# Kernel optimization log

Measured on AMD Instinct MI355X. Metric: run time of the kernel, lower is better.

Reference implementation:

```python
import jax, jax.numpy as jnp
import numpy as np

B, N, T = 64, 100, 100
FS, F, STRIDE = 3, 16, 1  # filter_size, num_filters, stride
DENSITY = 0.05


def setup_inputs() -> dict:
    key = jax.random.key(0)
    k1, k2, k3, k4 = jax.random.split(key, 4)
    vals = jax.random.uniform(k1, (B, N, N, T), dtype=jnp.float32, minval=0.01, maxval=1.0)
    mask = jax.random.uniform(k2, (B, N, N, T)) < DENSITY
    x = jnp.where(mask, vals, 0.0)
    # learned params, matching tf.random_normal_initializer(stddev=0.05)
    w = 0.05 * jax.random.normal(k3, (N * N * FS, F), dtype=jnp.float32)
    gammat = 0.05 * jax.random.normal(k4, (1, 1), dtype=jnp.float32)
    return {"x": x, "w": w, "gammat": gammat}


def reference(x, w, gammat):
    # gamma = (gamma_max - gamma_min) * sigmoid(gammat) + gamma_min, gamma_max=10
    gamma = 10.0 * jax.nn.sigmoid(gammat[0, 0])
    # tf.sparse.map_values(exp, -gamma*x): only nonzero entries are exponentiated
    xs = jnp.where(x != 0, jnp.exp(-gamma * x), 0.0)
    # windowed sparse-dense matmul over time == 1D conv over T with channels N*N
    xc = xs.reshape(B, N * N, T)                         # (B, NN, T)
    # w flattening order is ((i*N + j)*FS + dt) -> reshape (NN, FS, F)
    kern = w.reshape(N * N, FS, F).transpose(2, 0, 1)    # (F, NN, FS)
    out = jax.lax.conv_general_dilated(
        xc, kern, window_strides=(STRIDE,), padding="VALID",
        dimension_numbers=("NCH", "OIH", "NCH"))          # (B, F, T-FS+1)
    return out[:, :, None, :]                            # (B, F, 1, outT)
```

## Files before the change

kernel.cpp:

```cpp
#include <hip/hip_runtime.h>

#define BB     64
#define NNCH   10000
#define TT     100
#define TOUT   98
#define FF     16
#define CPB    64
#define NCHUNK 157
#define ETP    72
#define ETROWS 116
#define WP     200
#define ACCN   (TOUT * FF)

typedef __attribute__((ext_vector_type(8))) short s8v;
typedef __attribute__((ext_vector_type(4))) float f4v;

__device__ __forceinline__ ushort bf_rne(float v) {
    unsigned b = __float_as_uint(v);
    return (ushort)((b + 0x7FFFu + ((b >> 16) & 1u)) >> 16);
}

__global__ __launch_bounds__(256) void tgcnn_mfma(
    const float* __restrict__ x,
    const float* __restrict__ w,
    const float* __restrict__ gammat,
    float* __restrict__ ws)
{
    __shared__ __align__(16) ushort ET[ETROWS][ETP];
    __shared__ __align__(16) ushort W[FF][WP];

    const int tid = threadIdx.x;
    const int bid = blockIdx.x;
    const int b   = bid / NCHUNK;
    const int cs  = bid - b * NCHUNK;
    const int cbase = cs * CPB;

    const float gt    = gammat[0];
    const float gamma = 10.0f / (1.0f + __expf(-gt));
    const float kk    = -gamma * 1.4426950408889634f;

    {
        const uint4 z = make_uint4(0, 0, 0, 0);
        uint4* e4 = (uint4*)&ET[0][0];
        #pragma unroll
        for (int i = tid; i < (ETROWS * ETP * 2) / 16; i += 256) e4[i] = z;
        uint4* w4 = (uint4*)&W[0][0];
        for (int i = tid; i < (FF * WP * 2) / 16; i += 256) w4[i] = z;
    }
    __syncthreads();

    const float4* x4 = (const float4*)x;
    const int cl = tid & 63;
    const int c  = cbase + cl;
    const bool cok = (c < NNCH);
    const size_t xrow = ((size_t)b * NNCH + c) * 25;
    #pragma unroll
    for (int r = 0; r < 7; ++r) {
        const int q = r * 4 + (tid >> 6);
        if (q < 25 && cok) {
            float4 v = x4[xrow + q];
            const int t0 = q * 4;
            ET[t0 + 0][cl] = (v.x != 0.f) ? bf_rne(exp2f(kk * v.x)) : 0;
            ET[t0 + 1][cl] = (v.y != 0.f) ? bf_rne(exp2f(kk * v.y)) : 0;
            ET[t0 + 2][cl] = (v.z != 0.f) ? bf_rne(exp2f(kk * v.z)) : 0;
            ET[t0 + 3][cl] = (v.w != 0.f) ? bf_rne(exp2f(kk * v.w)) : 0;
        }
    }

    const float4* wg4 = (const float4*)w;
    if (tid < 192) {
        #pragma unroll
        for (int rr = 0; rr < 4; ++rr) {
            const int i  = rr * 192 + tid;
            const int wc = i / 12, r = i - wc * 12;
            if (cbase + wc < NNCH) {
                float4 wv = wg4[(size_t)(cbase + wc) * 12 + r];
                const int dt = r >> 2, fq = (r & 3) * 4;
                const int kp = dt * CPB + wc;
                W[fq + 0][kp] = bf_rne(wv.x);
                W[fq + 1][kp] = bf_rne(wv.y);
                W[fq + 2][kp] = bf_rne(wv.z);
                W[fq + 3][kp] = bf_rne(wv.w);
            }
        }
    }
    __syncthreads();

    const int wave = tid >> 6, lane = tid & 63;
    const int tcol = lane & 15;
    const int kb   = lane >> 4;
    const int tile0 = wave, tile1 = wave + 4;

    f4v acc0 = {0.f, 0.f, 0.f, 0.f};
    f4v acc1 = {0.f, 0.f, 0.f, 0.f};

    #pragma unroll
    for (int ks = 0; ks < 6; ++ks) {
        const int dt = ks >> 1;
        const int cb = (ks & 1) * 32 + kb * 8;

        s8v bfrag = *(const s8v*)&W[tcol][ks * 32 + kb * 8];

        const int trow0 = tile0 * 16 + tcol + dt;
        s8v a0 = *(const s8v*)&ET[trow0][cb];
        acc0 = __builtin_amdgcn_mfma_f32_16x16x32_bf16(a0, bfrag, acc0, 0, 0, 0);

        if (tile1 < 7) {
            const int trow1 = tile1 * 16 + tcol + dt;
            s8v a1 = *(const s8v*)&ET[trow1][cb];
            acc1 = __builtin_amdgcn_mfma_f32_16x16x32_bf16(a1, bfrag, acc1, 0, 0, 0);
        }
    }

    float* wsb = ws + (size_t)b * ACCN;
    const int f = lane & 15;
    const int rbase = (lane >> 4) * 4;
    #pragma unroll
    for (int r = 0; r < 4; ++r) {
        const int m = tile0 * 16 + rbase + r;
        if (m < TOUT) atomicAdd(&wsb[m * FF + f], acc0[r]);
    }
    if (tile1 < 7) {
        #pragma unroll
        for (int r = 0; r < 4; ++r) {
            const int m = tile1 * 16 + rbase + r;
            if (m < TOUT) atomicAdd(&wsb[m * FF + f], acc1[r]);
        }
    }
}

__global__ __launch_bounds__(256) void tgcnn_finalize(
    const float* __restrict__ ws, float* __restrict__ out)
{
    int i = blockIdx.x * 256 + threadIdx.x;
    if (i >= BB * FF * TOUT) return;
    int t = i % TOUT;
    int f = (i / TOUT) & (FF - 1);
    int b = i / (FF * TOUT);
    out[i] = ws[(size_t)b * ACCN + t * FF + f];
}

extern "C" void kernel_launch(void* const* d_in, const int* in_sizes, int n_in,
                              void* d_out, int out_size, void* d_ws, size_t ws_size,
                              hipStream_t stream) {
    const float* x = (const float*)d_in[0];
    const float* w = (const float*)d_in[1];
    const float* g = (const float*)d_in[2];
    float* ws = (float*)d_ws;

    hipMemsetAsync(d_ws, 0, (size_t)BB * ACCN * sizeof(float), stream);
    tgcnn_mfma<<<BB * NCHUNK, 256, 0, stream>>>(x, w, g, ws);
    tgcnn_finalize<<<(BB * FF * TOUT + 255) / 256, 256, 0, stream>>>(
        ws, (float*)d_out);
}
```

Baseline: 105.6 us.

## Loop each block over four channel chunks, swizzle LDS layout, atomically add into output

Each block now handles four 64-channel chunks in sequence and keeps its MFMA accumulators across them. This cuts the grid by roughly four times and the number of global atomics by the same factor. The exponentiated tile moves to an XOR-swizzled 8-channel-packed LDS layout with coalesced x loads (channel-major traversal) to cut bank conflicts. The finalize transpose kernel is dropped by atomically adding straight into the output in (f,t) order after a memset. The trade-off is fewer blocks to hide latency and per-chunk barriers that serialise load and compute within a block.

```diff
diff --git a/kernel.cpp b/kernel.cpp
--- a/kernel.cpp
+++ b/kernel.cpp
@@ -2,15 +2,14 @@
 
 #define BB     64
 #define NNCH   10000
-#define TT     100
 #define TOUT   98
 #define FF     16
 #define CPB    64
 #define NCHUNK 157
-#define ETP    72
-#define ETROWS 116
+#define CH     4
+#define NCO    40
+#define EROWS  128
 #define WP     200
-#define ACCN   (TOUT * FF)
 
 typedef __attribute__((ext_vector_type(8))) short s8v;
 typedef __attribute__((ext_vector_type(4))) float f4v;
@@ -20,124 +19,119 @@
     return (ushort)((b + 0x7FFFu + ((b >> 16) & 1u)) >> 16);
 }
 
+__device__ __forceinline__ int eaddr(int c, int t) {
+    int byte = ((c >> 3) << 11) | (t << 4) | ((c & 7) << 1);
+    return byte ^ (((t >> 2) & 3) << 5);
+}
+
 __global__ __launch_bounds__(256) void tgcnn_mfma(
     const float* __restrict__ x,
     const float* __restrict__ w,
     const float* __restrict__ gammat,
-    float* __restrict__ ws)
+    float* __restrict__ out)
 {
-    __shared__ __align__(16) ushort ET[ETROWS][ETP];
+    __shared__ __align__(16) ushort E8[8 * EROWS * 8];
     __shared__ __align__(16) ushort W[FF][WP];
 
     const int tid = threadIdx.x;
     const int bid = blockIdx.x;
-    const int b   = bid / NCHUNK;
-    const int cs  = bid - b * NCHUNK;
-    const int cbase = cs * CPB;
+    const int b   = bid / NCO;
+    const int co  = bid - b * NCO;
 
     const float gt    = gammat[0];
     const float gamma = 10.0f / (1.0f + __expf(-gt));
     const float kk    = -gamma * 1.4426950408889634f;
 
     {
-        const uint4 z = make_uint4(0, 0, 0, 0);
-        uint4* e4 = (uint4*)&ET[0][0];
+        uint4* e4 = (uint4*)E8;
         #pragma unroll
-        for (int i = tid; i < (ETROWS * ETP * 2) / 16; i += 256) e4[i] = z;
-        uint4* w4 = (uint4*)&W[0][0];
-        for (int i = tid; i < (FF * WP * 2) / 16; i += 256) w4[i] = z;
+        for (int i = tid; i < 1024; i += 256) e4[i] = make_uint4(0, 0, 0, 0);
     }
     __syncthreads();
 
-    const float4* x4 = (const float4*)x;
-    const int cl = tid & 63;
-    const int c  = cbase + cl;
-    const bool cok = (c < NNCH);
-    const size_t xrow = ((size_t)b * NNCH + c) * 25;
-    #pragma unroll
-    for (int r = 0; r < 7; ++r) {
-        const int q = r * 4 + (tid >> 6);
-        if (q < 25 && cok) {
-            float4 v = x4[xrow + q];
-            const int t0 = q * 4;
-            ET[t0 + 0][cl] = (v.x != 0.f) ? bf_rne(exp2f(kk * v.x)) : 0;
-            ET[t0 + 1][cl] = (v.y != 0.f) ? bf_rne(exp2f(kk * v.y)) : 0;
-            ET[t0 + 2][cl] = (v.z != 0.f) ? bf_rne(exp2f(kk * v.z)) : 0;
-            ET[t0 + 3][cl] = (v.w != 0.f) ? bf_rne(exp2f(kk * v.w)) : 0;
-        }
-    }
-
-    const float4* wg4 = (const float4*)w;
-    if (tid < 192) {
-        #pragma unroll
-        for (int rr = 0; rr < 4; ++rr) {
-            const int i  = rr * 192 + tid;
-            const int wc = i / 12, r = i - wc * 12;
-            if (cbase + wc < NNCH) {
-                float4 wv = wg4[(size_t)(cbase + wc) * 12 + r];
-                const int dt = r >> 2, fq = (r & 3) * 4;
-                const int kp = dt * CPB + wc;
-                W[fq + 0][kp] = bf_rne(wv.x);
-                W[fq + 1][kp] = bf_rne(wv.y);
-                W[fq + 2][kp] = bf_rne(wv.z);
-                W[fq + 3][kp] = bf_rne(wv.w);
-            }
-        }
-    }
-    __syncthreads();
-
-    const int wave = tid >> 6, lane = tid & 63;
-    const int tcol = lane & 15;
-    const int kb   = lane >> 4;
+    const int wave  = tid >> 6, lane = tid & 63;
+    const int tcol  = lane & 15;
+    const int kb    = lane >> 4;
     const int tile0 = wave, tile1 = wave + 4;
 
     f4v acc0 = {0.f, 0.f, 0.f, 0.f};
     f4v acc1 = {0.f, 0.f, 0.f, 0.f};
 
-    #pragma unroll
-    for (int ks = 0; ks < 6; ++ks) {
-        const int dt = ks >> 1;
-        const int cb = (ks & 1) * 32 + kb * 8;
+    const float4* x4  = (const float4*)x;
+    const float4* wg4 = (const float4*)w;
+    char* eb = (char*)E8;
 
-        s8v bfrag = *(const s8v*)&W[tcol][ks * 32 + kb * 8];
+    for (int kc = 0; kc < CH; ++kc) {
+        const int cs = co * CH + kc;
+        if (cs >= NCHUNK) break;
+        const int cbase = cs * CPB;
 
-        const int trow0 = tile0 * 16 + tcol + dt;
-        s8v a0 = *(const s8v*)&ET[trow0][cb];
-        acc0 = __builtin_amdgcn_mfma_f32_16x16x32_bf16(a0, bfrag, acc0, 0, 0, 0);
+        for (int r = 0; r < 7; ++r) {
+            const int i = r * 256 + tid;
+            if (i < 1600) {
+                const int cl = i / 25, q = i - cl * 25;
+                const int c  = cbase + cl;
+                float4 v = make_float4(0.f, 0.f, 0.f, 0.f);
+                if (c < NNCH) v = x4[((size_t)b * NNCH + c) * 25 + q];
+                const int t0 = q * 4;
+                ushort e0 = (v.x != 0.f) ? bf_rne(exp2f(kk * v.x)) : 0;
+                ushort e1 = (v.y != 0.f) ? bf_rne(exp2f(kk * v.y)) : 0;
+                ushort e2 = (v.z != 0.f) ? bf_rne(exp2f(kk * v.z)) : 0;
+                ushort e3 = (v.w != 0.f) ? bf_rne(exp2f(kk * v.w)) : 0;
+                *(ushort*)(eb + eaddr(cl, t0 + 0)) = e0;
+                *(ushort*)(eb + eaddr(cl, t0 + 1)) = e1;
+                *(ushort*)(eb + eaddr(cl, t0 + 2)) = e2;
+                *(ushort*)(eb + eaddr(cl, t0 + 3)) = e3;
+            }
+        }
 
-        if (tile1 < 7) {
-            const int trow1 = tile1 * 16 + tcol + dt;
-            s8v a1 = *(const s8v*)&ET[trow1][cb];
-            acc1 = __builtin_amdgcn_mfma_f32_16x16x32_bf16(a1, bfrag, acc1, 0, 0, 0);
+        for (int i = tid; i < 768; i += 256) {
+            const int wc = i / 12, r = i - wc * 12;
+            const int c  = cbase + wc;
+            float4 wv = make_float4(0.f, 0.f, 0.f, 0.f);
+            if (c < NNCH) wv = wg4[(size_t)c * 12 + r];
+            const int dt = r >> 2, fq = (r & 3) * 4, kp = dt * CPB + wc;
+            W[fq + 0][kp] = bf_rne(wv.x);
+            W[fq + 1][kp] = bf_rne(wv.y);
+            W[fq + 2][kp] = bf_rne(wv.z);
+            W[fq + 3][kp] = bf_rne(wv.w);
         }
+        __syncthreads();
+
+        #pragma unroll
+        for (int ks = 0; ks < 6; ++ks) {
+            const int dt = ks >> 1;
+            const int cb = (ks & 1) * 32 + kb * 8;
+            s8v bfrag = *(const s8v*)&W[tcol][ks * 32 + kb * 8];
+            {
+                const int trow = tile0 * 16 + tcol + dt;
+                s8v a0 = *(const s8v*)(eb + eaddr(cb, trow));
+                acc0 = __builtin_amdgcn_mfma_f32_16x16x32_bf16(a0, bfrag, acc0, 0, 0, 0);
+            }
+            if (tile1 < 7) {
+                const int trow = tile1 * 16 + tcol + dt;
+                s8v a1 = *(const s8v*)(eb + eaddr(cb, trow));
+                acc1 = __builtin_amdgcn_mfma_f32_16x16x32_bf16(a1, bfrag, acc1, 0, 0, 0);
+            }
+        }
+        __syncthreads();
     }
 
-    float* wsb = ws + (size_t)b * ACCN;
+    float* ob = out + (size_t)b * FF * TOUT;
     const int f = lane & 15;
     const int rbase = (lane >> 4) * 4;
     #pragma unroll
     for (int r = 0; r < 4; ++r) {
         const int m = tile0 * 16 + rbase + r;
-        if (m < TOUT) atomicAdd(&wsb[m * FF + f], acc0[r]);
+        if (m < TOUT) atomicAdd(&ob[f * TOUT + m], acc0[r]);
     }
     if (tile1 < 7) {
         #pragma unroll
         for (int r = 0; r < 4; ++r) {
             const int m = tile1 * 16 + rbase + r;
-            if (m < TOUT) atomicAdd(&wsb[m * FF + f], acc1[r]);
+            if (m < TOUT) atomicAdd(&ob[f * TOUT + m], acc1[r]);
         }
     }
-}
-
-__global__ __launch_bounds__(256) void tgcnn_finalize(
-    const float* __restrict__ ws, float* __restrict__ out)
-{
-    int i = blockIdx.x * 256 + threadIdx.x;
-    if (i >= BB * FF * TOUT) return;
-    int t = i % TOUT;
-    int f = (i / TOUT) & (FF - 1);
-    int b = i / (FF * TOUT);
-    out[i] = ws[(size_t)b * ACCN + t * FF + f];
 }
 
 extern "C" void kernel_launch(void* const* d_in, const int* in_sizes, int n_in,
@@ -146,10 +140,7 @@
     const float* x = (const float*)d_in[0];
     const float* w = (const float*)d_in[1];
     const float* g = (const float*)d_in[2];
-    float* ws = (float*)d_ws;
 
-    hipMemsetAsync(d_ws, 0, (size_t)BB * ACCN * sizeof(float), stream);
-    tgcnn_mfma<<<BB * NCHUNK, 256, 0, stream>>>(x, w, g, ws);
-    tgcnn_finalize<<<(BB * FF * TOUT + 255) / 256, 256, 0, stream>>>(
-        ws, (float*)d_out);
+    hipMemsetAsync(d_out, 0, (size_t)out_size * sizeof(float), stream);
+    tgcnn_mfma<<<BB * NCO, 256, 0, stream>>>(x, w, g, (float*)d_out);
 }
```

Measured after the change: 144.9 us. 1.37x slower.
